# Kernel optimization log

Hardware: AMD Instinct MI355X
Metric: run time of the kernel (lower is better)

The kernel has to match this reference:

```python
import jax, jax.numpy as jnp
import numpy as np

N_EMBED = 1024
NUM_HEADS = 16
HEAD_SIZE = 64  # NUM_HEADS * HEAD_SIZE == N_EMBED
BLOCK_SIZE = 2048


def setup_inputs() -> dict:
    key = jax.random.key(0)
    ks = jax.random.split(key, 9)
    s = 1.0 / np.sqrt(N_EMBED)
    batch_x = jax.random.normal(ks[0], (4, BLOCK_SIZE, N_EMBED), dtype=jnp.float32)
    # stacked per-head linear params: weight [H, E, d], bias [H, d]
    Wq = jax.random.uniform(ks[1], (NUM_HEADS, N_EMBED, HEAD_SIZE), jnp.float32, -s, s)
    Wk = jax.random.uniform(ks[2], (NUM_HEADS, N_EMBED, HEAD_SIZE), jnp.float32, -s, s)
    Wv = jax.random.uniform(ks[3], (NUM_HEADS, N_EMBED, HEAD_SIZE), jnp.float32, -s, s)
    bq = jax.random.uniform(ks[4], (NUM_HEADS, HEAD_SIZE), jnp.float32, -s, s)
    bk = jax.random.uniform(ks[5], (NUM_HEADS, HEAD_SIZE), jnp.float32, -s, s)
    bv = jax.random.uniform(ks[6], (NUM_HEADS, HEAD_SIZE), jnp.float32, -s, s)
    Wp = jax.random.uniform(ks[7], (N_EMBED, N_EMBED), jnp.float32, -s, s)
    bp = jax.random.uniform(ks[8], (N_EMBED,), jnp.float32, -s, s)
    return {"batch_x": batch_x, "Wq": Wq, "Wk": Wk, "Wv": Wv,
            "bq": bq, "bk": bk, "bv": bv, "Wp": Wp, "bp": bp}


def reference(batch_x, Wq, Wk, Wv, bq, bk, bv, Wp, bp):
    B, T, E = batch_x.shape
    # per-head projections: [B, H, T, d]
    q = jnp.einsum('bte,hed->bhtd', batch_x, Wq) + bq[None, :, None, :]
    k = jnp.einsum('bte,hed->bhtd', batch_x, Wk) + bk[None, :, None, :]
    v = jnp.einsum('bte,hed->bhtd', batch_x, Wv) + bv[None, :, None, :]
    scale = 1.0 / jnp.sqrt(jnp.asarray(HEAD_SIZE, batch_x.dtype))
    wei = jnp.einsum('bhtd,bhsd->bhts', q, k) * scale  # [B,H,T,T]
    causal = jnp.tril(jnp.ones((T, T), dtype=bool))
    wei = jnp.where(causal, wei, jnp.asarray(-jnp.inf, wei.dtype))
    wei = jax.nn.softmax(wei, axis=-1)
    out = jnp.einsum('bhts,bhsd->bhtd', wei, v)  # [B,H,T,d]
    # concat heads (head order matches torch.cat over ModuleList)
    out = out.transpose(0, 2, 1, 3).reshape(B, T, NUM_HEADS * HEAD_SIZE)
    return out @ Wp + bp
```

## Files before the change

### kernel.cpp

```cpp
#include <hip/hip_runtime.h>
#include <math.h>

#define B_ 4
#define T_ 2048
#define E_ 1024
#define H_ 16
#define D_ 64

typedef __bf16 bf16_t;
typedef bf16_t bf16x8 __attribute__((ext_vector_type(8)));
typedef float  f32x4  __attribute__((ext_vector_type(4)));
typedef float  f32x16 __attribute__((ext_vector_type(16)));
typedef unsigned short u16x4 __attribute__((ext_vector_type(4)));
typedef unsigned int   u32x4 __attribute__((ext_vector_type(4)));

static __device__ __forceinline__ unsigned short f2bf(float f) {
    bf16_t h = (bf16_t)f;
    return __builtin_bit_cast(unsigned short, h);
}
static __device__ __forceinline__ unsigned int pk2(float a, float b) {
    return (unsigned int)f2bf(a) | ((unsigned int)f2bf(b) << 16);
}

#define GLD(gp, lp) __builtin_amdgcn_global_load_lds( \
    (const __attribute__((address_space(1))) unsigned int*)(gp), \
    (__attribute__((address_space(3))) unsigned int*)(lp), 16, 0, 0)

#define BAR() __builtin_amdgcn_s_barrier()
#define WAIT_LGKM0() asm volatile("s_waitcnt lgkmcnt(0)" ::: "memory")

__global__ void cast_x_kernel(const float* __restrict__ in, unsigned short* __restrict__ out, int n4) {
    int i = blockIdx.x * blockDim.x + threadIdx.x;
    if (i >= n4) return;
    float4 v = ((const float4*)in)[i];
    ushort4 o;
    o.x = f2bf(v.x); o.y = f2bf(v.y); o.z = f2bf(v.z); o.w = f2bf(v.w);
    ((ushort4*)out)[i] = o;
}

__global__ void tcast_all(const float* __restrict__ Wq, const float* __restrict__ Wk,
                          const float* __restrict__ Wv, const float* __restrict__ Wp,
                          unsigned short* __restrict__ wf, unsigned short* __restrict__ wpt) {
    __shared__ unsigned short Ts[64 * 66];
    const int grp = blockIdx.y >> 4, yy = blockIdx.y & 15;
    const float* in; unsigned short* out; int yA, S;
    if (grp == 3) { in = Wp; out = wpt; yA = 64;    S = 1024; }
    else {
        in = (grp == 0) ? Wq : (grp == 1) ? Wk : Wv;
        out = wf + (size_t)grp * 1024 * 1024; yA = 65536; S = 64;
    }
    const int tid = threadIdx.x;
    const int r = tid >> 2, c4 = tid & 3;
    const float* ip = in + (size_t)yA * yy + (size_t)(blockIdx.x * 64 + r) * S + c4 * 16;
    #pragma unroll
    for (int j = 0; j < 4; ++j) {
        float4 v = *(const float4*)&ip[j * 4];
        Ts[(c4 * 16 + j * 4 + 0) * 66 + r] = f2bf(v.x);
        Ts[(c4 * 16 + j * 4 + 1) * 66 + r] = f2bf(v.y);
        Ts[(c4 * 16 + j * 4 + 2) * 66 + r] = f2bf(v.z);
        Ts[(c4 * 16 + j * 4 + 3) * 66 + r] = f2bf(v.w);
    }
    __syncthreads();
    unsigned short* op = out + (size_t)(yy * 64 + r) * 1024 + blockIdx.x * 64 + c4 * 16;
    #pragma unroll
    for (int j = 0; j < 4; ++j) {
        u16x4 pk;
        #pragma unroll
        for (int m = 0; m < 4; ++m) pk[m] = Ts[r * 66 + c4 * 16 + j * 4 + m];
        *(u16x4*)&op[j * 4] = pk;
    }
}

__global__ __launch_bounds__(512, 2) void qkv_gemm(
    const unsigned short* __restrict__ xb,
    const unsigned short* __restrict__ wf,
    const float* __restrict__ bq, const float* __restrict__ bk, const float* __restrict__ bv,
    unsigned short* __restrict__ qo, unsigned short* __restrict__ ko,
    unsigned short* __restrict__ vt)
{
    __shared__ __align__(16) unsigned short sm[65536];

    const int tid = threadIdx.x;
    const int w = tid >> 6, lane = tid & 63;
    const int wr = w >> 2, wc = w & 3;
    const int l15 = lane & 15, quad = lane >> 4, lsw = l15 & 7;
    const int m0 = blockIdx.x * 256;
    const int n0 = blockIdx.y * 256;

    f32x4 acc[8][4];
    #pragma unroll
    for (int i = 0; i < 8; ++i)
        #pragma unroll
        for (int j = 0; j < 4; ++j) acc[i][j] = (f32x4){0.f, 0.f, 0.f, 0.f};

    const int swzE = (((lane & 7) ^ (lane >> 3)) * 8);
    const unsigned short* Agb = xb + (size_t)(m0 + w * 16 + (lane >> 3)) * 1024 + swzE;
    const unsigned short* Bgb = wf + (size_t)(n0 + w * 16 + (lane >> 3)) * 1024 + swzE;

    auto stage_half = [&](int t, int which) {
        unsigned short* dst = sm + (t & 1) * 32768 + which * 8192 + w * 1024;
        const unsigned short* src = ((which < 2) ? Agb : Bgb)
                                  + (size_t)((which & 1) * 128) * 1024 + t * 64;
        GLD(src, dst);
        GLD(src + (size_t)8 * 1024, dst + 512);
    };
    auto rdA = [&](int t, int fm, int ks) {
        const int row = wr * 128 + fm * 16 + l15;
        return *(const bf16x8*)&sm[(t & 1) * 32768 + (row >> 7) * 8192
                                   + (row & 127) * 64 + (((ks * 4 + quad) ^ lsw) * 8)];
    };
    auto rdB = [&](int t, int fn, int ks) {
        const int row = wc * 64 + fn * 16 + l15;
        return *(const bf16x8*)&sm[(t & 1) * 32768 + 16384 + (row >> 7) * 8192
                                   + (row & 127) * 64 + (((ks * 4 + quad) ^ lsw) * 8)];
    };

    stage_half(0, 0); stage_half(0, 1); stage_half(0, 2); stage_half(0, 3);
    stage_half(1, 2); stage_half(1, 3);
    asm volatile("s_waitcnt vmcnt(4)" ::: "memory");
    BAR();

    #define MFMA_Q(mb, nb) \
        __builtin_amdgcn_s_setprio(1); \
        _Pragma("unroll") \
        for (int i_ = 0; i_ < 4; ++i_) \
            _Pragma("unroll") \
            for (int j_ = 0; j_ < 2; ++j_) \
                _Pragma("unroll") \
                for (int ks_ = 0; ks_ < 2; ++ks_) \
                    acc[(mb) + i_][(nb) + j_] = __builtin_amdgcn_mfma_f32_16x16x32_bf16( \
                        fA[i_][ks_], fB[(nb) + j_][ks_], acc[(mb) + i_][(nb) + j_], 0, 0, 0); \
        __builtin_amdgcn_s_setprio(0);

    #pragma unroll 1
    for (int it = 0; it < 8; ++it) {
        const int t0 = 2 * it, t1 = 2 * it + 1;
        const bool more = it < 7;
        bf16x8 fA[4][2], fB[4][2];

        #pragma unroll
        for (int m = 0; m < 4; ++m) { fA[m][0] = rdA(t0, m, 0); fA[m][1] = rdA(t0, m, 1); }
        #pragma unroll
        for (int n = 0; n < 2; ++n) { fB[n][0] = rdB(t0, n, 0); fB[n][1] = rdB(t0, n, 1); }
        stage_half(t1, 0);
        BAR(); WAIT_LGKM0();
        MFMA_Q(0, 0);
        BAR();

        #pragma unroll
        for (int n = 0; n < 2; ++n) { fB[2 + n][0] = rdB(t0, 2 + n, 0); fB[2 + n][1] = rdB(t0, 2 + n, 1); }
        stage_half(t1, 1);
        BAR(); WAIT_LGKM0();
        MFMA_Q(0, 2);
        BAR();

        #pragma unroll
        for (int m = 0; m < 4; ++m) { fA[m][0] = rdA(t0, 4 + m, 0); fA[m][1] = rdA(t0, 4 + m, 1); }
        if (more) stage_half(t0 + 2, 2);
        BAR(); WAIT_LGKM0();
        MFMA_Q(4, 2);
        BAR();

        if (more) {
            stage_half(t0 + 2, 3);
            asm volatile("s_waitcnt vmcnt(4)" ::: "memory");
        } else {
            asm volatile("s_waitcnt vmcnt(0)" ::: "memory");
        }
        BAR();
        MFMA_Q(4, 0);
        BAR();

        #pragma unroll
        for (int m = 0; m < 4; ++m) { fA[m][0] = rdA(t1, m, 0); fA[m][1] = rdA(t1, m, 1); }
        #pragma unroll
        for (int n = 0; n < 2; ++n) { fB[n][0] = rdB(t1, n, 0); fB[n][1] = rdB(t1, n, 1); }
        if (more) stage_half(t0 + 2, 0);
        BAR(); WAIT_LGKM0();
        MFMA_Q(0, 0);
        BAR();

        #pragma unroll
        for (int n = 0; n < 2; ++n) { fB[2 + n][0] = rdB(t1, 2 + n, 0); fB[2 + n][1] = rdB(t1, 2 + n, 1); }
        if (more) stage_half(t0 + 2, 1);
        BAR(); WAIT_LGKM0();
        MFMA_Q(0, 2);
        BAR();

        #pragma unroll
        for (int m = 0; m < 4; ++m) { fA[m][0] = rdA(t1, 4 + m, 0); fA[m][1] = rdA(t1, 4 + m, 1); }
        if (more) stage_half(t1 + 2, 2);
        BAR(); WAIT_LGKM0();
        MFMA_Q(4, 2);
        BAR();

        if (more) {
            stage_half(t1 + 2, 3);
            asm volatile("s_waitcnt vmcnt(4)" ::: "memory");
        } else {
            asm volatile("s_waitcnt vmcnt(0)" ::: "memory");
        }
        BAR();
        MFMA_Q(4, 0);
        BAR();
    }
    #undef MFMA_Q

    const int which = n0 >> 10;
    const int nb = n0 & 1023;
    if (which < 2) {
        const float* bias = which ? bk : bq;
        unsigned short* outp = which ? ko : qo;
        const float sc = which ? 1.f : 0.125f;
        #pragma unroll
        for (int fm = 0; fm < 8; ++fm)
            #pragma unroll
            for (int fn = 0; fn < 4; ++fn) {
                int colg = nb + wc * 64 + fn * 16 + l15;
                int h = colg >> 6, d = colg & 63;
                float bi = bias[colg];
                #pragma unroll
                for (int r = 0; r < 4; ++r) {
                    int row = m0 + wr * 128 + fm * 16 + quad * 4 + r;
                    int b = row >> 11, t = row & 2047;
                    outp[(((size_t)b * 16 + h) * 2048 + t) * 64 + d] = f2bf((acc[fm][fn][r] + bi) * sc);
                }
            }
    } else {
        const int b = m0 >> 11;
        for (int mh = 0; mh < 2; ++mh)
            for (int nh = 0; nh < 2; ++nh) {
                __syncthreads();
                if (wr == mh && (wc >> 1) == nh) {
                    const int cc = wc & 1;
                    #pragma unroll
                    for (int fm = 0; fm < 8; ++fm)
                        #pragma unroll
                        for (int fn = 0; fn < 4; ++fn) {
                            int colL = cc * 64 + fn * 16 + l15;
                            int colg = nb + nh * 128 + colL;
                            float bi = bv[colg];
                            u16x4 pk;
                            #pragma unroll
                            for (int r = 0; r < 4; ++r) pk[r] = f2bf(acc[fm][fn][r] + bi);
                            *(u16x4*)&sm[colL * 136 + fm * 16 + quad * 4] = pk;
                        }
                }
                __syncthreads();
                const int nl = tid >> 2, tq = tid & 3;
                const int colg = nb + nh * 128 + nl;
                const int h = colg >> 6, d = colg & 63;
                const int t0 = (m0 & 2047) + mh * 128;
                unsigned short* dst = vt + (((size_t)b * 16 + h) * 64 + d) * 2048 + t0 + tq * 32;
                #pragma unroll
                for (int j = 0; j < 4; ++j)
                    *(float4*)&dst[j * 8] = *(const float4*)&sm[nl * 136 + tq * 32 + j * 8];
            }
    }
}

__global__ __launch_bounds__(256, 4) void attn_kernel(
    const unsigned short* __restrict__ q, const unsigned short* __restrict__ k,
    const unsigned short* __restrict__ vt, unsigned short* __restrict__ att2)
{
    __shared__ __align__(16) unsigned short KV[2][2][4096];

    const int tid = threadIdx.x;
    const int w = tid >> 6, lane = tid & 63;
    const int l31 = lane & 31, h = lane >> 5;
    const int bh = blockIdx.x;
    const int rs = l31 & 7;

    const unsigned short* kb = k  + (size_t)bh * 2048 * 64;
    const unsigned short* vb = vt + (size_t)bh * 64 * 2048;

    const int swz = ((lane & 7) ^ (lane >> 3)) * 8;
    const unsigned short* Kg = kb + (size_t)(16 * w + (lane >> 3)) * 64 + swz;
    const unsigned short* Vg = vb + (size_t)(16 * w + (lane >> 3)) * 2048 + swz;

    for (int leg = 0; leg < 2; ++leg) {
        const int qtile = leg ? (15 - (int)blockIdx.y) : (int)blockIdx.y;
        const int qb0 = qtile * 128;
        const int qmin = qb0 + w * 32, qmax = qmin + 31;
        const int qg = qmin + l31;
        const int trips = 2 * qtile + 2;

        bf16x8 fQ[4];
        {
            const unsigned short* qp = q + ((size_t)bh * 2048 + qg) * 64 + h * 8;
            #pragma unroll
            for (int ks = 0; ks < 4; ++ks) fQ[ks] = *(const bf16x8*)&qp[ks * 16];
        }

        f32x16 O[2];
        #pragma unroll
        for (int nt = 0; nt < 2; ++nt)
            #pragma unroll
            for (int i = 0; i < 16; ++i) O[nt][i] = 0.f;
        float lsum = 0.f;

        {
            unsigned short* dK = &KV[0][0][w * 1024];
            unsigned short* dV = &KV[0][1][w * 1024];
            GLD(Kg, dK); GLD(Kg + 512, dK + 512);
            GLD(Vg, dV); GLD(Vg + 8 * 2048, dV + 512);
        }
        asm volatile("s_waitcnt vmcnt(0)" ::: "memory");
        BAR();

        for (int jt = 0; jt < trips; ++jt) {
            const int buf = jt & 1;
            if (jt + 1 < trips) {
                unsigned short* dK = &KV[buf ^ 1][0][w * 1024];
                unsigned short* dV = &KV[buf ^ 1][1][w * 1024];
                const unsigned short* sK = Kg + (size_t)(jt + 1) * 4096;
                const unsigned short* sV = Vg + (jt + 1) * 64;
                GLD(sK, dK); GLD(sK + 512, dK + 512);
                GLD(sV, dV); GLD(sV + 8 * 2048, dV + 512);
            }
            const unsigned short* Ks = KV[buf][0];
            const unsigned short* Vs = KV[buf][1];

            const int key0 = jt * 64;
            if (key0 <= qmax) {
                f32x16 S[2];
                #pragma unroll
                for (int kt = 0; kt < 2; ++kt)
                    #pragma unroll
                    for (int i = 0; i < 16; ++i) S[kt][i] = 0.f;
                __builtin_amdgcn_s_setprio(1);
                #pragma unroll
                for (int kt = 0; kt < 2; ++kt) {
                    const int row = kt * 32 + l31;
                    #pragma unroll
                    for (int ks = 0; ks < 4; ++ks) {
                        bf16x8 aK = *(const bf16x8*)&Ks[row * 64 + ((2 * ks + h) ^ rs) * 8];
                        S[kt] = __builtin_amdgcn_mfma_f32_32x32x16_bf16(aK, fQ[ks], S[kt], 0, 0, 0);
                    }
                }
                __builtin_amdgcn_s_setprio(0);

                const bool need_mask = (key0 + 63) > qmin;
                unsigned int e0[2][4], e1[2][4];
                #pragma unroll
                for (int kt = 0; kt < 2; ++kt)
                    #pragma unroll
                    for (int g = 0; g < 4; ++g) {
                        float p[4];
                        #pragma unroll
                        for (int r = 0; r < 4; ++r) {
                            float pv = __expf(S[kt][4 * g + r]);
                            if (need_mask) {
                                int key = key0 + kt * 32 + 8 * g + 4 * h + r;
                                if (key > qg) pv = 0.f;
                            }
                            p[r] = pv;
                            lsum += pv;
                        }
                        e0[kt][g] = pk2(p[0], p[1]);
                        e1[kt][g] = pk2(p[2], p[3]);
                    }

                __builtin_amdgcn_s_setprio(1);
                #pragma unroll
                for (int ks2 = 0; ks2 < 4; ++ks2) {
                    const int kt = ks2 >> 1, s = ks2 & 1;
                    const int ge = 2 * s, go = 2 * s + 1;
                    unsigned int own0 = h ? e0[kt][go] : e0[kt][ge];
                    unsigned int snd0 = h ? e0[kt][ge] : e0[kt][go];
                    unsigned int rcv0 = (unsigned int)__shfl_xor((int)snd0, 32);
                    unsigned int own1 = h ? e1[kt][go] : e1[kt][ge];
                    unsigned int snd1 = h ? e1[kt][ge] : e1[kt][go];
                    unsigned int rcv1 = (unsigned int)__shfl_xor((int)snd1, 32);
                    u32x4 t;
                    t[0] = h ? rcv0 : own0;
                    t[1] = h ? rcv1 : own1;
                    t[2] = h ? own0 : rcv0;
                    t[3] = h ? own1 : rcv1;
                    bf16x8 aP = __builtin_bit_cast(bf16x8, t);
                    #pragma unroll
                    for (int nt = 0; nt < 2; ++nt) {
                        const int drow = nt * 32 + l31;
                        bf16x8 bV = *(const bf16x8*)&Vs[drow * 64 + ((2 * ks2 + h) ^ rs) * 8];
                        O[nt] = __builtin_amdgcn_mfma_f32_32x32x16_bf16(aP, bV, O[nt], 0, 0, 0);
                    }
                }
                __builtin_amdgcn_s_setprio(0);
            }

            asm volatile("s_waitcnt vmcnt(0)" ::: "memory");
            BAR();
        }

        lsum += __shfl_xor(lsum, 32);
        const float inv = 1.f / lsum;

        unsigned short* ob = att2 + ((size_t)bh * 2048 + qmin) * 64;
        #pragma unroll
        for (int g = 0; g < 4; ++g)
            #pragma unroll
            for (int r = 0; r < 4; ++r) {
                const int qy = 8 * g + 4 * h + r;
                const float iv = __shfl(inv, qy);
                #pragma unroll
                for (int nt = 0; nt < 2; ++nt)
                    ob[(size_t)qy * 64 + nt * 32 + l31] = f2bf(O[nt][4 * g + r] * iv);
            }
    }
}

__global__ __launch_bounds__(256) void proj_gemm(
    const unsigned short* __restrict__ A,
    const unsigned short* __restrict__ wpt,
    const float* __restrict__ bp,
    float* __restrict__ out)
{
    __shared__ __align__(16) unsigned short sm[16384];
    unsigned short* As = sm;
    unsigned short* Bs = sm + 8192;

    const int tid = threadIdx.x;
    const int w = tid >> 6, lane = tid & 63, l15 = lane & 15, quad = lane >> 4;
    const int m0 = blockIdx.x * 128;
    const int n0 = blockIdx.y * 128;

    f32x4 acc[2][8];
    #pragma unroll
    for (int s = 0; s < 2; ++s)
        #pragma unroll
        for (int n = 0; n < 8; ++n) acc[s][n] = (f32x4){0.f, 0.f, 0.f, 0.f};

    const unsigned short* Ag = A + (size_t)(m0 >> 11) * 16 * 131072
                                 + (size_t)((m0 & 2047) + 32 * w + (lane >> 3)) * 64 + (lane & 7) * 8;
    const unsigned short* Bg = wpt + (size_t)(n0 + 32 * w + (lane >> 3)) * 1024 + (lane & 7) * 8;
    unsigned short* Al = As + (32 * w) * 64;
    unsigned short* Bl = Bs + (32 * w) * 64;

    for (int k0 = 0; k0 < 1024; k0 += 64) {
        __syncthreads();
        const size_t aoff = (size_t)(k0 >> 6) * 131072;
        #pragma unroll
        for (int j = 0; j < 4; ++j) {
            GLD(Ag + aoff + (size_t)(8 * j) * 64, Al + (8 * j) * 64);
            GLD(Bg + (size_t)(8 * j) * 1024 + k0, Bl + (8 * j) * 64);
        }
        __syncthreads();
        #pragma unroll
        for (int ks = 0; ks < 2; ++ks) {
            bf16x8 a0 = *(const bf16x8*)&As[(32 * w + l15) * 64 + ks * 32 + quad * 8];
            bf16x8 a1 = *(const bf16x8*)&As[(32 * w + 16 + l15) * 64 + ks * 32 + quad * 8];
            #pragma unroll
            for (int n = 0; n < 8; ++n) {
                bf16x8 b = *(const bf16x8*)&Bs[(16 * n + l15) * 64 + ks * 32 + quad * 8];
                acc[0][n] = __builtin_amdgcn_mfma_f32_16x16x32_bf16(a0, b, acc[0][n], 0, 0, 0);
                acc[1][n] = __builtin_amdgcn_mfma_f32_16x16x32_bf16(a1, b, acc[1][n], 0, 0, 0);
            }
        }
    }

    #pragma unroll
    for (int s = 0; s < 2; ++s)
        #pragma unroll
        for (int n = 0; n < 8; ++n) {
            float bi = bp[n0 + 16 * n + l15];
            #pragma unroll
            for (int r = 0; r < 4; ++r) {
                int row = m0 + 32 * w + 16 * s + quad * 4 + r;
                out[(size_t)row * 1024 + n0 + 16 * n + l15] = acc[s][n][r] + bi;
            }
        }
}

extern "C" void kernel_launch(void* const* d_in, const int* in_sizes, int n_in,
                              void* d_out, int out_size, void* d_ws, size_t ws_size,
                              hipStream_t stream) {
    const float* x  = (const float*)d_in[0];
    const float* Wq = (const float*)d_in[1];
    const float* Wk = (const float*)d_in[2];
    const float* Wv = (const float*)d_in[3];
    const float* bq = (const float*)d_in[4];
    const float* bk = (const float*)d_in[5];
    const float* bv = (const float*)d_in[6];
    const float* Wp = (const float*)d_in[7];
    const float* bp = (const float*)d_in[8];
    float* out = (float*)d_out;

    const size_t nx = (size_t)B_ * T_ * E_;
    unsigned short* base = (unsigned short*)d_ws;
    unsigned short* xb  = base;
    unsigned short* qb  = xb + nx;
    unsigned short* kb  = qb + nx;
    unsigned short* vtb = kb + nx;
    unsigned short* atb = vtb + nx;
    unsigned short* wf  = atb + nx;
    unsigned short* wpt = wf + 3072 * 1024;

    cast_x_kernel<<<(int)(nx / 4 + 255) / 256, 256, 0, stream>>>(x, xb, (int)(nx / 4));
    tcast_all<<<dim3(16, 64), 256, 0, stream>>>(Wq, Wk, Wv, Wp, wf, wpt);
    qkv_gemm<<<dim3(32, 12), 512, 0, stream>>>(xb, wf, bq, bk, bv, qb, kb, vtb);
    attn_kernel<<<dim3(64, 8), 256, 0, stream>>>(qb, kb, vtb, atb);
    proj_gemm<<<dim3(64, 8), 256, 0, stream>>>(atb, wpt, bp, out);
}
```

Baseline: 276.8 us.

## Use 128-key attention tiles, exp2 with folded log2e, permlane32 swap, split accumulators

The attention key/value tile grows from 64 to 128 keys, which halves the number of loop trips and barriers per query tile; launch bounds drop to 2 blocks per CU to make room for the larger LDS. The log2(e) factor is folded into the Q scaling so the softmax can use raw v_exp_f32. The cross-half P shuffle is replaced with v_permlane32_swap, and two O accumulators alternate to break MFMA dependency chains. The costs are more registers and LDS, lower occupancy, and causal skipping done per 32-key sub-block inside a coarser tile.

```diff
diff --git a/kernel.cpp b/kernel.cpp
--- a/kernel.cpp
+++ b/kernel.cpp
@@ -20,6 +20,12 @@
 }
 static __device__ __forceinline__ unsigned int pk2(float a, float b) {
     return (unsigned int)f2bf(a) | ((unsigned int)f2bf(b) << 16);
+}
+static __device__ __forceinline__ float ex2(float x) {
+    float r; asm("v_exp_f32 %0, %1" : "=v"(r) : "v"(x)); return r;
+}
+static __device__ __forceinline__ void pl32swap(unsigned int& a, unsigned int& b) {
+    asm("v_permlane32_swap_b32 %0, %1" : "+v"(a), "+v"(b));
 }
 
 #define GLD(gp, lp) __builtin_amdgcn_global_load_lds( \
@@ -211,7 +217,7 @@
     if (which < 2) {
         const float* bias = which ? bk : bq;
         unsigned short* outp = which ? ko : qo;
-        const float sc = which ? 1.f : 0.125f;
+        const float sc = which ? 1.f : 0.125f * 1.44269504088896f;
         #pragma unroll
         for (int fm = 0; fm < 8; ++fm)
             #pragma unroll
@@ -259,31 +265,45 @@
     }
 }
 
-__global__ __launch_bounds__(256, 4) void attn_kernel(
+__global__ __launch_bounds__(256, 2) void attn_kernel(
     const unsigned short* __restrict__ q, const unsigned short* __restrict__ k,
     const unsigned short* __restrict__ vt, unsigned short* __restrict__ att2)
 {
-    __shared__ __align__(16) unsigned short KV[2][2][4096];
+    __shared__ __align__(16) unsigned short KV[2][2][8192];
 
     const int tid = threadIdx.x;
     const int w = tid >> 6, lane = tid & 63;
     const int l31 = lane & 31, h = lane >> 5;
     const int bh = blockIdx.x;
-    const int rs = l31 & 7;
+    const int rs = l31 & 7, rv = l31 & 15;
 
     const unsigned short* kb = k  + (size_t)bh * 2048 * 64;
     const unsigned short* vb = vt + (size_t)bh * 64 * 2048;
 
-    const int swz = ((lane & 7) ^ (lane >> 3)) * 8;
-    const unsigned short* Kg = kb + (size_t)(16 * w + (lane >> 3)) * 64 + swz;
-    const unsigned short* Vg = vb + (size_t)(16 * w + (lane >> 3)) * 2048 + swz;
+    const size_t kOff = (size_t)(32 * w + (lane >> 3)) * 64 + (size_t)(((lane & 7) ^ (lane >> 3)) * 8);
+    const int vRow = lane >> 4, vc = lane & 15;
+    size_t vOff[4];
+    #pragma unroll
+    for (int r = 0; r < 4; ++r)
+        vOff[r] = (size_t)(16 * w + 4 * r + vRow) * 2048
+                + (size_t)((vc ^ ((4 * r + vRow) & 15)) * 8);
+
+    auto stage = [&](int jt, int buf) {
+        unsigned short* dK = &KV[buf][0][w * 2048];
+        unsigned short* dV = &KV[buf][1][w * 2048];
+        const unsigned short* sK = kb + kOff + (size_t)jt * 8192;
+        #pragma unroll
+        for (int r = 0; r < 4; ++r) GLD(sK + r * 512, dK + r * 512);
+        #pragma unroll
+        for (int r = 0; r < 4; ++r) GLD(vb + vOff[r] + jt * 128, dV + r * 512);
+    };
 
     for (int leg = 0; leg < 2; ++leg) {
         const int qtile = leg ? (15 - (int)blockIdx.y) : (int)blockIdx.y;
         const int qb0 = qtile * 128;
         const int qmin = qb0 + w * 32, qmax = qmin + 31;
         const int qg = qmin + l31;
-        const int trips = 2 * qtile + 2;
+        const int trips = qtile + 1;
 
         bf16x8 fQ[4];
         {
@@ -292,100 +312,89 @@
             for (int ks = 0; ks < 4; ++ks) fQ[ks] = *(const bf16x8*)&qp[ks * 16];
         }
 
-        f32x16 O[2];
+        f32x16 Oa[2], Ob[2];
         #pragma unroll
         for (int nt = 0; nt < 2; ++nt)
             #pragma unroll
-            for (int i = 0; i < 16; ++i) O[nt][i] = 0.f;
+            for (int i = 0; i < 16; ++i) { Oa[nt][i] = 0.f; Ob[nt][i] = 0.f; }
         float lsum = 0.f;
 
-        {
-            unsigned short* dK = &KV[0][0][w * 1024];
-            unsigned short* dV = &KV[0][1][w * 1024];
-            GLD(Kg, dK); GLD(Kg + 512, dK + 512);
-            GLD(Vg, dV); GLD(Vg + 8 * 2048, dV + 512);
-        }
+        stage(0, 0);
         asm volatile("s_waitcnt vmcnt(0)" ::: "memory");
         BAR();
 
         for (int jt = 0; jt < trips; ++jt) {
             const int buf = jt & 1;
-            if (jt + 1 < trips) {
-                unsigned short* dK = &KV[buf ^ 1][0][w * 1024];
-                unsigned short* dV = &KV[buf ^ 1][1][w * 1024];
-                const unsigned short* sK = Kg + (size_t)(jt + 1) * 4096;
-                const unsigned short* sV = Vg + (jt + 1) * 64;
-                GLD(sK, dK); GLD(sK + 512, dK + 512);
-                GLD(sV, dV); GLD(sV + 8 * 2048, dV + 512);
-            }
+            if (jt + 1 < trips) stage(jt + 1, buf ^ 1);
             const unsigned short* Ks = KV[buf][0];
             const unsigned short* Vs = KV[buf][1];
-
-            const int key0 = jt * 64;
-            if (key0 <= qmax) {
-                f32x16 S[2];
+            const int key0 = jt * 128;
+
+            f32x16 S[4];
+            #pragma unroll
+            for (int kt = 0; kt < 4; ++kt)
                 #pragma unroll
-                for (int kt = 0; kt < 2; ++kt)
-                    #pragma unroll
-                    for (int i = 0; i < 16; ++i) S[kt][i] = 0.f;
-                __builtin_amdgcn_s_setprio(1);
-                #pragma unroll
-                for (int kt = 0; kt < 2; ++kt) {
+                for (int i = 0; i < 16; ++i) S[kt][i] = 0.f;
+            __builtin_amdgcn_s_setprio(1);
+            #pragma unroll
+            for (int kt = 0; kt < 4; ++kt) {
+                if (key0 + 32 * kt <= qmax) {
                     const int row = kt * 32 + l31;
                     #pragma unroll
                     for (int ks = 0; ks < 4; ++ks) {
-                        bf16x8 aK = *(const bf16x8*)&Ks[row * 64 + ((2 * ks + h) ^ rs) * 8];
+                        bf16x8 aK = *(const bf16x8*)&Ks[row * 64 + (((2 * ks + h) ^ rs) * 8)];
                         S[kt] = __builtin_amdgcn_mfma_f32_32x32x16_bf16(aK, fQ[ks], S[kt], 0, 0, 0);
                     }
                 }
-                __builtin_amdgcn_s_setprio(0);
-
-                const bool need_mask = (key0 + 63) > qmin;
-                unsigned int e0[2][4], e1[2][4];
-                #pragma unroll
-                for (int kt = 0; kt < 2; ++kt)
+            }
+            __builtin_amdgcn_s_setprio(0);
+
+            #pragma unroll
+            for (int kt = 0; kt < 4; ++kt) {
+                if (key0 + 32 * kt <= qmax) {
+                    const bool nm = (key0 + 32 * kt + 31) > qmin;
+                    unsigned int e0[4], e1[4];
+                    float lst = 0.f;
                     #pragma unroll
                     for (int g = 0; g < 4; ++g) {
                         float p[4];
                         #pragma unroll
                         for (int r = 0; r < 4; ++r) {
-                            float pv = __expf(S[kt][4 * g + r]);
-                            if (need_mask) {
+                            float pv = ex2(S[kt][4 * g + r]);
+                            if (nm) {
                                 int key = key0 + kt * 32 + 8 * g + 4 * h + r;
                                 if (key > qg) pv = 0.f;
                             }
                             p[r] = pv;
-                            lsum += pv;
                         }
-                        e0[kt][g] = pk2(p[0], p[1]);
-                        e1[kt][g] = pk2(p[2], p[3]);
+                        lst += (p[0] + p[1]) + (p[2] + p[3]);
+                        e0[g] = pk2(p[0], p[1]);
+                        e1[g] = pk2(p[2], p[3]);
                     }
-
-                __builtin_amdgcn_s_setprio(1);
-                #pragma unroll
-                for (int ks2 = 0; ks2 < 4; ++ks2) {
-                    const int kt = ks2 >> 1, s = ks2 & 1;
-                    const int ge = 2 * s, go = 2 * s + 1;
-                    unsigned int own0 = h ? e0[kt][go] : e0[kt][ge];
-                    unsigned int snd0 = h ? e0[kt][ge] : e0[kt][go];
-                    unsigned int rcv0 = (unsigned int)__shfl_xor((int)snd0, 32);
-                    unsigned int own1 = h ? e1[kt][go] : e1[kt][ge];
-                    unsigned int snd1 = h ? e1[kt][ge] : e1[kt][go];
-                    unsigned int rcv1 = (unsigned int)__shfl_xor((int)snd1, 32);
-                    u32x4 t;
-                    t[0] = h ? rcv0 : own0;
-                    t[1] = h ? rcv1 : own1;
-                    t[2] = h ? own0 : rcv0;
-                    t[3] = h ? own1 : rcv1;
-                    bf16x8 aP = __builtin_bit_cast(bf16x8, t);
+                    lsum += lst;
+
+                    __builtin_amdgcn_s_setprio(1);
                     #pragma unroll
-                    for (int nt = 0; nt < 2; ++nt) {
-                        const int drow = nt * 32 + l31;
-                        bf16x8 bV = *(const bf16x8*)&Vs[drow * 64 + ((2 * ks2 + h) ^ rs) * 8];
-                        O[nt] = __builtin_amdgcn_mfma_f32_32x32x16_bf16(aP, bV, O[nt], 0, 0, 0);
+                    for (int s = 0; s < 2; ++s) {
+                        unsigned int a = e0[2 * s], b = e0[2 * s + 1];
+                        pl32swap(a, b);
+                        unsigned int c2 = e1[2 * s], d2 = e1[2 * s + 1];
+                        pl32swap(c2, d2);
+                        u32x4 t; t[0] = a; t[1] = c2; t[2] = b; t[3] = d2;
+                        bf16x8 aP = __builtin_bit_cast(bf16x8, t);
+                        const int cb = 4 * kt + 2 * s;
+                        #pragma unroll
+                        for (int nt = 0; nt < 2; ++nt) {
+                            const int drow = nt * 32 + l31;
+                            bf16x8 bV = *(const bf16x8*)&Vs[drow * 128 + (((cb + h) ^ rv) * 8)];
+                            if (kt & 1)
+                                Ob[nt] = __builtin_amdgcn_mfma_f32_32x32x16_bf16(aP, bV, Ob[nt], 0, 0, 0);
+                            else
+                                Oa[nt] = __builtin_amdgcn_mfma_f32_32x32x16_bf16(aP, bV, Oa[nt], 0, 0, 0);
+                        }
                     }
+                    __builtin_amdgcn_s_setprio(0);
                 }
-                __builtin_amdgcn_s_setprio(0);
             }
 
             asm volatile("s_waitcnt vmcnt(0)" ::: "memory");
@@ -404,7 +413,8 @@
                 const float iv = __shfl(inv, qy);
                 #pragma unroll
                 for (int nt = 0; nt < 2; ++nt)
-                    ob[(size_t)qy * 64 + nt * 32 + l31] = f2bf(O[nt][4 * g + r] * iv);
+                    ob[(size_t)qy * 64 + nt * 32 + l31] =
+                        f2bf((Oa[nt][4 * g + r] + Ob[nt][4 * g + r]) * iv);
             }
     }
 }
```

After: 269.6 us. 1.03x faster.
